# Kernel tuning notes

Measured on AMD Instinct MI355X. Metric: run time of the kernel, lower is better.

## Reference

```python
import jax, jax.numpy as jnp
import numpy as np

N = 30000          # nodes
E = 480000         # directed edges (avg degree 16)
F_IN = 376         # num_features (hard-coded in module)
HID = 512          # nhid (hard-coded)
NEG_SLOPE = 0.2    # PyG GATConv default negative_slope


def _lin(k, fi, fo):
    return (jax.random.normal(k, (fi, fo), jnp.float32) / np.sqrt(fi)).astype(jnp.float32)


def setup_inputs() -> dict:
    key = jax.random.key(0)
    ks = jax.random.split(key, 16)
    d = {}
    d["x"] = jax.random.normal(ks[0], (N, F_IN), jnp.float32)
    d["edge_index"] = jax.random.randint(ks[1], (2, E), 0, N)
    d["edge_weight"] = jax.random.uniform(ks[2], (E,), jnp.float32)
    # GCNConv(376,512) and GCNConv(512,512)
    d["W1"] = _lin(ks[3], F_IN, HID); d["b1"] = jnp.zeros((HID,), jnp.float32)
    d["W2"] = _lin(ks[4], HID, HID);  d["b2"] = jnp.zeros((HID,), jnp.float32)
    # SAGEConv(512,512): lin_l on aggregated neighbors, lin_r on root
    d["sage_Wl"] = _lin(ks[5], HID, HID)
    d["sage_Wr"] = _lin(ks[6], HID, HID)
    d["sage_b"] = jnp.zeros((HID,), jnp.float32)
    # GATConv(1536, 1, heads=4, concat=False)
    d["gat1_W"] = _lin(ks[7], 3 * HID, 4)
    d["gat1_a_src"] = jax.random.normal(ks[8], (4,), jnp.float32) * 0.1
    d["gat1_a_dst"] = jax.random.normal(ks[9], (4,), jnp.float32) * 0.1
    d["gat1_b"] = jnp.zeros((1,), jnp.float32)
    # GATConv(1536, 1, heads=16, concat=False)
    d["gat2_W"] = _lin(ks[10], 3 * HID, 16)
    d["gat2_a_src"] = jax.random.normal(ks[11], (16,), jnp.float32) * 0.1
    d["gat2_a_dst"] = jax.random.normal(ks[12], (16,), jnp.float32) * 0.1
    d["gat2_b"] = jnp.zeros((1,), jnp.float32)
    return d


def gcn_conv(x, src, dst, ew, W, b, n):
    # PyG GCNConv: add self-loops (weight 1), symmetric normalization
    loop = jnp.arange(n)
    s = jnp.concatenate([src, loop])
    t = jnp.concatenate([dst, loop])
    w = jnp.concatenate([ew, jnp.ones((n,), ew.dtype)])
    deg = jax.ops.segment_sum(w, t, num_segments=n)
    dinv = jnp.where(deg > 0, jax.lax.rsqrt(deg), 0.0)
    norm = dinv[s] * w * dinv[t]                       # [E+N]
    h = x @ W                                           # [N, out]
    out = jax.ops.segment_sum(norm[:, None] * h[s], t, num_segments=n)
    return out + b


def sage_conv(x, src, dst, Wl, Wr, b, n):
    # PyG SAGEConv: mean neighbor aggregation + root transform
    sums = jax.ops.segment_sum(x[src], dst, num_segments=n)
    cnt = jax.ops.segment_sum(jnp.ones((src.shape[0],), x.dtype), dst, num_segments=n)
    mean = sums / jnp.maximum(cnt, 1.0)[:, None]
    return mean @ Wl + x @ Wr + b


def gat_conv(x, src, dst, W, a_src, a_dst, b, n):
    # PyG GATConv (out_channels=1, concat=False -> mean over heads), self-loops added
    loop = jnp.arange(n)
    s = jnp.concatenate([src, loop])
    t = jnp.concatenate([dst, loop])
    h = x @ W                                           # [N, heads] (C=1)
    e = jax.nn.leaky_relu(h[s] * a_src + h[t] * a_dst, NEG_SLOPE)  # [E+N, heads]
    m = jax.ops.segment_max(e, t, num_segments=n)       # stable segment softmax
    ex = jnp.exp(e - m[t])
    den = jax.ops.segment_sum(ex, t, num_segments=n)
    alpha = ex / den[t]
    out = jax.ops.segment_sum(alpha * h[s], t, num_segments=n)     # [N, heads]
    return out.mean(axis=1, keepdims=True) + b          # [N, 1]


def reference(x, edge_index, edge_weight, W1, b1, W2, b2,
              sage_Wl, sage_Wr, sage_b,
              gat1_W, gat1_a_src, gat1_a_dst, gat1_b,
              gat2_W, gat2_a_src, gat2_a_dst, gat2_b):
    n = x.shape[0]
    src, dst = edge_index[0], edge_index[1]
    x1 = jax.nn.relu(gcn_conv(x, src, dst, edge_weight, W1, b1, n))
    x2 = jax.nn.relu(gcn_conv(x1, src, dst, edge_weight, W2, b2, n))
    x3 = jax.nn.relu(sage_conv(x1, src, dst, sage_Wl, sage_Wr, sage_b, n))
    dense_features = jnp.concatenate([x1, x2, x3], axis=1)  # [N, 1536]
    a1 = gat_conv(dense_features, src, dst, gat1_W, gat1_a_src, gat1_a_dst, gat1_b, n)
    a2 = gat_conv(dense_features, src, dst, gat2_W, gat2_a_src, gat2_a_dst, gat2_b, n)
    x_out = jnp.ravel((a1 + a2) * 0.5)                  # [N]
    return x_out, dense_features
```

## Files before the change

kernel.cpp:

```cpp
#include <hip/hip_runtime.h>
#include <hip/hip_bf16.h>
#include <stdint.h>

#define N_NODES 30000
#define M_PAD   30080
#define N_EDGES 480000
#define F_IN 376
#define K1   384
#define HID 512
#define DENSE_F 1536
#define NHEADS 20
#define HG_LD 128

typedef __bf16 bf16_t;
typedef bf16_t bf16x8 __attribute__((ext_vector_type(8)));
typedef bf16_t bf16x4 __attribute__((ext_vector_type(4)));
typedef float  f32x4  __attribute__((ext_vector_type(4)));

__global__ __launch_bounds__(256) void build_stats(
    const int* __restrict__ dst, const float* __restrict__ ew,
    float* __restrict__ deg, int* __restrict__ cnt)
{
    int e = blockIdx.x * 256 + threadIdx.x;
    if (e >= N_EDGES) return;
    int t = dst[e];
    atomicAdd(&deg[t], ew[e]);
    atomicAdd(&cnt[t], 1);
}

__global__ __launch_bounds__(256) void node_stats(
    float* __restrict__ deg, float* __restrict__ dinv)
{
    int i = blockIdx.x * 256 + threadIdx.x;
    if (i >= N_NODES) return;
    float d = deg[i] + 1.0f;
    deg[i] = d;
    dinv[i] = rsqrtf(d);
}

__global__ __launch_bounds__(1024) void scan_rowptr(
    const int* __restrict__ cnt, int* __restrict__ rowptr, int* __restrict__ woff)
{
    __shared__ int temp[1024];
    __shared__ int carry;
    int t = threadIdx.x;
    if (t == 0) carry = 0;
    __syncthreads();
    for (int base = 0; base < N_NODES; base += 1024) {
        int i = base + t;
        int v = (i < N_NODES) ? cnt[i] : 0;
        temp[t] = v;
        __syncthreads();
        for (int off = 1; off < 1024; off <<= 1) {
            int add = (t >= off) ? temp[t - off] : 0;
            __syncthreads();
            temp[t] += add;
            __syncthreads();
        }
        int excl = temp[t] - v;
        if (i < N_NODES) { rowptr[i] = carry + excl; woff[i] = carry + excl; }
        __syncthreads();
        if (t == 1023) carry += temp[1023];
        __syncthreads();
    }
    if (t == 0) rowptr[N_NODES] = carry;
}

__global__ __launch_bounds__(256) void scatter_csr(
    const int* __restrict__ src, const int* __restrict__ dst,
    const float* __restrict__ ew, int* __restrict__ woff,
    int* __restrict__ col, float* __restrict__ wcsr)
{
    int e = blockIdx.x * 256 + threadIdx.x;
    if (e >= N_EDGES) return;
    int t = dst[e];
    int p = atomicAdd(&woff[t], 1);
    col[p] = src[e];
    wcsr[p] = ew[e];
}

__global__ __launch_bounds__(256) void conv_x(
    const float* __restrict__ x, bf16_t* __restrict__ xb)
{
    int tid = blockIdx.x * 256 + threadIdx.x;
    if (tid >= M_PAD * K1) return;
    int r = tid / K1, c = tid - r * K1;
    float v = (r < N_NODES && c < F_IN) ? x[r * F_IN + c] : 0.f;
    xb[tid] = (bf16_t)v;
}

#define S1 (512 * K1)
#define S2 (512 * 512)
#define S3 (512 * 1024)
#define S4 (HG_LD * DENSE_F)
__global__ __launch_bounds__(256) void pack_weights(
    const float* __restrict__ W1, const float* __restrict__ W2,
    const float* __restrict__ Wl, const float* __restrict__ Wr,
    const float* __restrict__ g1W, const float* __restrict__ g2W,
    const float* __restrict__ a1s, const float* __restrict__ a1d,
    const float* __restrict__ a2s, const float* __restrict__ a2d,
    bf16_t* __restrict__ W1t, bf16_t* __restrict__ W2t,
    bf16_t* __restrict__ Bst, bf16_t* __restrict__ Wgt,
    float* __restrict__ asrc, float* __restrict__ adst)
{
    int tid = blockIdx.x * 256 + threadIdx.x;
    if (tid < S1) {
        int n = tid / K1, k = tid - n * K1;
        W1t[tid] = (bf16_t)((k < F_IN) ? W1[k * HID + n] : 0.f);
    } else if (tid < S1 + S2) {
        int t = tid - S1;
        int n = t >> 9, k = t & 511;
        W2t[t] = (bf16_t)W2[k * HID + n];
    } else if (tid < S1 + S2 + S3) {
        int t = tid - S1 - S2;
        int n = t >> 10, k = t & 1023;
        Bst[t] = (bf16_t)((k < HID) ? Wl[k * HID + n] : Wr[(k - HID) * HID + n]);
    } else if (tid < S1 + S2 + S3 + S4) {
        int t = tid - S1 - S2 - S3;
        int n = t / DENSE_F, k = t - n * DENSE_F;
        float v = (n < 4) ? g1W[k * 4 + n] : (n < NHEADS) ? g2W[k * 16 + (n - 4)] : 0.f;
        Wgt[t] = (bf16_t)v;
    } else if (tid < S1 + S2 + S3 + S4 + NHEADS) {
        int hh = tid - S1 - S2 - S3 - S4;
        asrc[hh] = (hh < 4) ? a1s[hh] : a2s[hh - 4];
        adst[hh] = (hh < 4) ? a1d[hh] : a2d[hh - 4];
    }
}

__global__ __launch_bounds__(256) void gemm_bf16(
    const bf16_t* __restrict__ A1, int lda1, int ksplit,
    const bf16_t* __restrict__ A2, int lda2,
    const bf16_t* __restrict__ Bt, int ldb,
    float* __restrict__ C, bf16_t* __restrict__ Cb, long ldc, int K)
{
    __shared__ bf16_t As[128 * 32];
    __shared__ bf16_t Bs[128 * 32];
    const int tid = threadIdx.x;
    const int wid = tid >> 6, lane = tid & 63;
    const int li = lane & 15, kq = lane >> 4;
    const int wm = (wid >> 1) * 64, wn = (wid & 1) * 64;
    const long r0 = (long)blockIdx.y * 128;
    const long n0 = (long)blockIdx.x * 128;

    f32x4 acc[4][4] = {};

    const int s0 = wid * 64 + lane;
    const int s1 = 256 + s0;
    const int am0 = s0 >> 2, ak0 = (s0 & 3) ^ ((am0 >> 1) & 3);
    const int am1 = s1 >> 2, ak1 = (s1 & 3) ^ ((am1 >> 1) & 3);
    const int swz = (li >> 1) & 3;

    for (int k0 = 0; k0 < K; k0 += 32) {
        const bf16_t* Ab; int lda;
        if (k0 < ksplit) { Ab = A1 + k0;            lda = lda1; }
        else             { Ab = A2 + (k0 - ksplit); lda = lda2; }
        __builtin_amdgcn_global_load_lds(
            (const __attribute__((address_space(1))) void*)(Ab + (r0 + am0) * (long)lda + ak0 * 8),
            (__attribute__((address_space(3))) void*)(As + (wid * 64) * 8), 16, 0, 0);
        __builtin_amdgcn_global_load_lds(
            (const __attribute__((address_space(1))) void*)(Ab + (r0 + am1) * (long)lda + ak1 * 8),
            (__attribute__((address_space(3))) void*)(As + (256 + wid * 64) * 8), 16, 0, 0);
        __builtin_amdgcn_global_load_lds(
            (const __attribute__((address_space(1))) void*)(Bt + (n0 + am0) * (long)ldb + k0 + ak0 * 8),
            (__attribute__((address_space(3))) void*)(Bs + (wid * 64) * 8), 16, 0, 0);
        __builtin_amdgcn_global_load_lds(
            (const __attribute__((address_space(1))) void*)(Bt + (n0 + am1) * (long)ldb + k0 + ak1 * 8),
            (__attribute__((address_space(3))) void*)(Bs + (256 + wid * 64) * 8), 16, 0, 0);
        __syncthreads();

        bf16x8 a[4], b[4];
#pragma unroll
        for (int f = 0; f < 4; ++f) {
            int m = wm + f * 16 + li;
            a[f] = *(const bf16x8*)(As + m * 32 + ((kq ^ swz) * 8));
            int n = wn + f * 16 + li;
            b[f] = *(const bf16x8*)(Bs + n * 32 + ((kq ^ swz) * 8));
        }
#pragma unroll
        for (int fm = 0; fm < 4; ++fm)
#pragma unroll
            for (int fn = 0; fn < 4; ++fn)
                acc[fm][fn] = __builtin_amdgcn_mfma_f32_16x16x32_bf16(
                    a[fm], b[fn], acc[fm][fn], 0, 0, 0);
        __syncthreads();
    }

    if (Cb) {
#pragma unroll
        for (int fm = 0; fm < 4; ++fm)
#pragma unroll
            for (int r = 0; r < 4; ++r) {
                long row = r0 + wm + fm * 16 + kq * 4 + r;
                bf16_t* cp = Cb + row * ldc + n0 + wn + li;
#pragma unroll
                for (int fn = 0; fn < 4; ++fn)
                    cp[fn * 16] = (bf16_t)acc[fm][fn][r];
            }
    } else {
#pragma unroll
        for (int fm = 0; fm < 4; ++fm)
#pragma unroll
            for (int r = 0; r < 4; ++r) {
                long row = r0 + wm + fm * 16 + kq * 4 + r;
                float* cp = C + row * ldc + n0 + wn + li;
#pragma unroll
                for (int fn = 0; fn < 4; ++fn)
                    cp[fn * 16] = acc[fm][fn][r];
            }
    }
}

__global__ __launch_bounds__(64) void gcn_agg(
    const bf16_t* __restrict__ hb, const int* __restrict__ rowptr,
    const int* __restrict__ col, const float* __restrict__ wcsr,
    const float* __restrict__ dinv, const float* __restrict__ deg,
    const float* __restrict__ bias, float* __restrict__ out,
    bf16_t* __restrict__ outb)
{
    int i = blockIdx.x;
    int c = threadIdx.x * 8;
    float di = dinv[i];
    float selfw = 1.0f / deg[i];
    bf16x8 sv = *(const bf16x8*)(hb + (long)i * HID + c);
    float acc0[8], acc1[8];
#pragma unroll
    for (int j = 0; j < 8; ++j) { acc0[j] = selfw * (float)sv[j]; acc1[j] = 0.f; }
    int e = rowptr[i], e1 = rowptr[i + 1];
    for (; e + 1 < e1; e += 2) {
        int sA = col[e], sB = col[e + 1];
        float wA = dinv[sA] * wcsr[e] * di;
        float wB = dinv[sB] * wcsr[e + 1] * di;
        bf16x8 vA = *(const bf16x8*)(hb + (long)sA * HID + c);
        bf16x8 vB = *(const bf16x8*)(hb + (long)sB * HID + c);
#pragma unroll
        for (int j = 0; j < 8; ++j) {
            acc0[j] = fmaf(wA, (float)vA[j], acc0[j]);
            acc1[j] = fmaf(wB, (float)vB[j], acc1[j]);
        }
    }
    if (e < e1) {
        int sA = col[e];
        float wA = dinv[sA] * wcsr[e] * di;
        bf16x8 vA = *(const bf16x8*)(hb + (long)sA * HID + c);
#pragma unroll
        for (int j = 0; j < 8; ++j) acc0[j] = fmaf(wA, (float)vA[j], acc0[j]);
    }
    float o[8];
#pragma unroll
    for (int j = 0; j < 8; ++j)
        o[j] = fmaxf(acc0[j] + acc1[j] + bias[c + j], 0.f);
    float* op = out + (long)i * DENSE_F + c;
    *reinterpret_cast<float4*>(op)     = make_float4(o[0], o[1], o[2], o[3]);
    *reinterpret_cast<float4*>(op + 4) = make_float4(o[4], o[5], o[6], o[7]);
    bf16x8 ob;
#pragma unroll
    for (int j = 0; j < 8; ++j) ob[j] = (bf16_t)o[j];
    *reinterpret_cast<bf16x8*>(outb + (long)i * DENSE_F + c) = ob;
}

__global__ __launch_bounds__(64) void sage_mean(
    const bf16_t* __restrict__ x1b, const int* __restrict__ rowptr,
    const int* __restrict__ col, const int* __restrict__ cnt,
    bf16_t* __restrict__ meanb)
{
    int i = blockIdx.x;
    int c = threadIdx.x * 8;
    float acc0[8] = {}, acc1[8] = {};
    int e = rowptr[i], e1 = rowptr[i + 1];
    for (; e + 1 < e1; e += 2) {
        int sA = col[e], sB = col[e + 1];
        bf16x8 vA = *(const bf16x8*)(x1b + (long)sA * DENSE_F + c);
        bf16x8 vB = *(const bf16x8*)(x1b + (long)sB * DENSE_F + c);
#pragma unroll
        for (int j = 0; j < 8; ++j) {
            acc0[j] += (float)vA[j];
            acc1[j] += (float)vB[j];
        }
    }
    if (e < e1) {
        int sA = col[e];
        bf16x8 vA = *(const bf16x8*)(x1b + (long)sA * DENSE_F + c);
#pragma unroll
        for (int j = 0; j < 8; ++j) acc0[j] += (float)vA[j];
    }
    float inv = 1.0f / fmaxf((float)cnt[i], 1.0f);
    bf16x8 ob;
#pragma unroll
    for (int j = 0; j < 8; ++j) ob[j] = (bf16_t)((acc0[j] + acc1[j]) * inv);
    *reinterpret_cast<bf16x8*>(meanb + (long)i * HID + c) = ob;
}

__global__ __launch_bounds__(256) void sage_finish(
    const float* __restrict__ h, const float* __restrict__ bias,
    float* __restrict__ out, bf16_t* __restrict__ outb)
{
    int tid = blockIdx.x * 256 + threadIdx.x;
    if (tid >= N_NODES * HID) return;
    int i = tid >> 9;
    int c = tid & (HID - 1);
    float v = fmaxf(h[tid] + bias[c], 0.f);
    out[(long)i * DENSE_F + c] = v;
    outb[(long)i * DENSE_F + c] = (bf16_t)v;
}

__global__ __launch_bounds__(64) void gat_agg(
    const float* __restrict__ hgat, const int* __restrict__ rowptr,
    const int* __restrict__ col, const float* __restrict__ asrc,
    const float* __restrict__ adst, const float* __restrict__ b1p,
    const float* __restrict__ b2p, float* __restrict__ xout)
{
    int i = blockIdx.x;
    int lane = threadIdx.x;
    int h = (lane < NHEADS) ? lane : 0;
    float hg_i = hgat[(long)i * HG_LD + h];
    float as = asrc[h], ad = adst[h];
    float adhg = ad * hg_i;
    float ev = hg_i * as + adhg;
    ev = ev > 0.f ? ev : 0.2f * ev;
    float ex = __expf(ev);
    float den = ex, og = ex * hg_i;
    int e0 = rowptr[i], e1 = rowptr[i + 1];
    for (int e = e0; e < e1; ++e) {
        int s = col[e];
        float hs = hgat[(long)s * HG_LD + h];
        float t = fmaf(hs, as, adhg);
        t = t > 0.f ? t : 0.2f * t;
        float x = __expf(t);
        den += x;
        og = fmaf(x, hs, og);
    }
    float out = (lane < NHEADS) ? og / den : 0.f;
    float s4 = out + __shfl_xor(out, 1);
    s4 += __shfl_xor(s4, 2);
    float g0 = __shfl(s4, 0);
    float g1 = __shfl(s4, 4);
    float g2 = __shfl(s4, 8);
    float g3 = __shfl(s4, 12);
    float g4 = __shfl(s4, 16);
    if (lane == 0) {
        float a1 = g0 * 0.25f + b1p[0];
        float a2 = (g1 + g2 + g3 + g4) * 0.0625f + b2p[0];
        xout[i] = 0.5f * (a1 + a2);
    }
}

extern "C" void kernel_launch(void* const* d_in, const int* in_sizes, int n_in,
                              void* d_out, int out_size, void* d_ws, size_t ws_size,
                              hipStream_t stream) {
    (void)in_sizes; (void)n_in; (void)out_size; (void)ws_size;
    const float* x    = (const float*)d_in[0];
    const int*   ei   = (const int*)d_in[1];
    const float* ew   = (const float*)d_in[2];
    const float* W1   = (const float*)d_in[3];
    const float* b1   = (const float*)d_in[4];
    const float* W2   = (const float*)d_in[5];
    const float* b2   = (const float*)d_in[6];
    const float* sWl  = (const float*)d_in[7];
    const float* sWr  = (const float*)d_in[8];
    const float* sb   = (const float*)d_in[9];
    const float* g1W  = (const float*)d_in[10];
    const float* g1as = (const float*)d_in[11];
    const float* g1ad = (const float*)d_in[12];
    const float* g1b  = (const float*)d_in[13];
    const float* g2W  = (const float*)d_in[14];
    const float* g2as = (const float*)d_in[15];
    const float* g2ad = (const float*)d_in[16];
    const float* g2b  = (const float*)d_in[17];

    const int* src = ei;
    const int* dst = ei + N_EDGES;

    float* xout  = (float*)d_out;
    float* dense = xout + N_NODES;

    size_t off = 0;
    auto alloc = [&](size_t nbytes) -> void* {
        void* p = (char*)d_ws + off;
        off += (nbytes + 255) & ~(size_t)255;
        return p;
    };
    float*  h        = (float*)alloc((size_t)M_PAD * HID * 4);
    bf16_t* h_bf     = (bf16_t*)h;
    bf16_t* dense_bf = (bf16_t*)alloc((size_t)M_PAD * DENSE_F * 2);
    bf16_t* x_bf     = (bf16_t*)alloc((size_t)M_PAD * K1 * 2);
    bf16_t* mean_bf  = (bf16_t*)alloc((size_t)M_PAD * HID * 2);
    bf16_t* W1t      = (bf16_t*)alloc((size_t)512 * K1 * 2);
    bf16_t* W2t      = (bf16_t*)alloc((size_t)512 * 512 * 2);
    bf16_t* Bst      = (bf16_t*)alloc((size_t)512 * 1024 * 2);
    bf16_t* Wgt      = (bf16_t*)alloc((size_t)HG_LD * DENSE_F * 2);
    float*  deg      = (float*)alloc((size_t)N_NODES * 4);
    float*  dinv     = (float*)alloc((size_t)N_NODES * 4);
    float*  asrc     = (float*)alloc(32 * 4);
    float*  adst     = (float*)alloc(32 * 4);
    int*    cnt      = (int*)alloc((size_t)N_NODES * 4);
    int*    rowp     = (int*)alloc((size_t)(N_NODES + 1) * 4);
    int*    woff     = (int*)alloc((size_t)N_NODES * 4);
    int*    colx     = (int*)alloc((size_t)N_EDGES * 4);
    float*  wcsr     = (float*)alloc((size_t)N_EDGES * 4);
    float*  hgat     = h;

    const int EB = (N_EDGES + 255) / 256;
    const int NB = (N_NODES + 255) / 256;

    hipMemsetAsync(deg, 0, (size_t)N_NODES * 4, stream);
    hipMemsetAsync(cnt, 0, (size_t)N_NODES * 4, stream);
    build_stats<<<EB, 256, 0, stream>>>(dst, ew, deg, cnt);
    node_stats<<<NB, 256, 0, stream>>>(deg, dinv);
    scan_rowptr<<<1, 1024, 0, stream>>>(cnt, rowp, woff);
    scatter_csr<<<EB, 256, 0, stream>>>(src, dst, ew, woff, colx, wcsr);

    conv_x<<<(M_PAD * K1 + 255) / 256, 256, 0, stream>>>(x, x_bf);
    pack_weights<<<(S1 + S2 + S3 + S4 + NHEADS + 255) / 256, 256, 0, stream>>>(
        W1, W2, sWl, sWr, g1W, g2W, g1as, g1ad, g2as, g2ad,
        W1t, W2t, Bst, Wgt, asrc, adst);

    const dim3 gB(256);
    const dim3 g512(HID / 128, M_PAD / 128);
    const dim3 g128(1, M_PAD / 128);

    gemm_bf16<<<g512, gB, 0, stream>>>(x_bf, K1, K1, x_bf, K1, W1t, K1,
                                       nullptr, h_bf, HID, K1);
    gcn_agg<<<N_NODES, 64, 0, stream>>>(h_bf, rowp, colx, wcsr, dinv, deg, b1,
                                        dense, dense_bf);
    gemm_bf16<<<g512, gB, 0, stream>>>(dense_bf, DENSE_F, HID, dense_bf, DENSE_F,
                                       W2t, HID, nullptr, h_bf, HID, HID);
    gcn_agg<<<N_NODES, 64, 0, stream>>>(h_bf, rowp, colx, wcsr, dinv, deg, b2,
                                        dense + HID, dense_bf + HID);
    sage_mean<<<N_NODES, 64, 0, stream>>>(dense_bf, rowp, colx, cnt, mean_bf);
    gemm_bf16<<<g512, gB, 0, stream>>>(mean_bf, HID, HID, dense_bf, DENSE_F,
                                       Bst, 1024, h, nullptr, HID, 1024);
    sage_finish<<<(N_NODES * HID + 255) / 256, 256, 0, stream>>>(
        h, sb, dense + 2 * HID, dense_bf + 2 * HID);

    gemm_bf16<<<g128, gB, 0, stream>>>(dense_bf, DENSE_F, DENSE_F, dense_bf, DENSE_F,
                                       Wgt, DENSE_F, hgat, nullptr, HG_LD, DENSE_F);
    gat_agg<<<N_NODES, 64, 0, stream>>>(hgat, rowp, colx, asrc, adst, g1b, g2b, xout);
}
```

Before: 871.2 us.

## Aggregate before transform in GCN layers and fuse bias/ReLU into GEMM epilogue

Result: faster. 802.8 us (-7.8%).

```diff
diff --git a/kernel.cpp b/kernel.cpp
--- a/kernel.cpp
+++ b/kernel.cpp
@@ -10,11 +10,10 @@
 #define HID 512
 #define DENSE_F 1536
 #define NHEADS 20
-#define HG_LD 128
+#define HG_LD 32
 
 typedef __bf16 bf16_t;
 typedef bf16_t bf16x8 __attribute__((ext_vector_type(8)));
-typedef bf16_t bf16x4 __attribute__((ext_vector_type(4)));
 typedef float  f32x4  __attribute__((ext_vector_type(4)));
 
 __global__ __launch_bounds__(256) void build_stats(
@@ -92,7 +91,7 @@
 #define S1 (512 * K1)
 #define S2 (512 * 512)
 #define S3 (512 * 1024)
-#define S4 (HG_LD * DENSE_F)
+#define S4 (128 * DENSE_F)
 __global__ __launch_bounds__(256) void pack_weights(
     const float* __restrict__ W1, const float* __restrict__ W2,
     const float* __restrict__ Wl, const float* __restrict__ Wr,
@@ -131,7 +130,8 @@
     const bf16_t* __restrict__ A1, int lda1, int ksplit,
     const bf16_t* __restrict__ A2, int lda2,
     const bf16_t* __restrict__ Bt, int ldb,
-    float* __restrict__ C, bf16_t* __restrict__ Cb, long ldc, int K)
+    float* __restrict__ C, bf16_t* __restrict__ Cb, long ldc, int K,
+    const float* __restrict__ bias, int ncols)
 {
     __shared__ bf16_t As[128 * 32];
     __shared__ bf16_t Bs[128 * 32];
@@ -140,7 +140,7 @@
     const int li = lane & 15, kq = lane >> 4;
     const int wm = (wid >> 1) * 64, wn = (wid & 1) * 64;
     const long r0 = (long)blockIdx.y * 128;
-    const long n0 = (long)blockIdx.x * 128;
+    const int  n0 = blockIdx.x * 128;
 
     f32x4 acc[4][4] = {};
 
@@ -185,122 +185,128 @@
         __syncthreads();
     }
 
-    if (Cb) {
-#pragma unroll
-        for (int fm = 0; fm < 4; ++fm)
-#pragma unroll
-            for (int r = 0; r < 4; ++r) {
-                long row = r0 + wm + fm * 16 + kq * 4 + r;
-                bf16_t* cp = Cb + row * ldc + n0 + wn + li;
-#pragma unroll
-                for (int fn = 0; fn < 4; ++fn)
-                    cp[fn * 16] = (bf16_t)acc[fm][fn][r];
+#pragma unroll
+    for (int fm = 0; fm < 4; ++fm) {
+#pragma unroll
+        for (int r = 0; r < 4; ++r) {
+            long row = r0 + wm + fm * 16 + kq * 4 + r;
+            if (row >= N_NODES) continue;
+#pragma unroll
+            for (int fn = 0; fn < 4; ++fn) {
+                int colg = n0 + wn + fn * 16 + li;
+                if (colg >= ncols) continue;
+                float v = acc[fm][fn][r];
+                if (bias) v = fmaxf(v + bias[colg], 0.f);
+                if (C)  C[row * ldc + colg]  = v;
+                if (Cb) Cb[row * ldc + colg] = (bf16_t)v;
             }
-    } else {
-#pragma unroll
-        for (int fm = 0; fm < 4; ++fm)
-#pragma unroll
-            for (int r = 0; r < 4; ++r) {
-                long row = r0 + wm + fm * 16 + kq * 4 + r;
-                float* cp = C + row * ldc + n0 + wn + li;
-#pragma unroll
-                for (int fn = 0; fn < 4; ++fn)
-                    cp[fn * 16] = acc[fm][fn][r];
-            }
-    }
-}
-
-__global__ __launch_bounds__(64) void gcn_agg(
-    const bf16_t* __restrict__ hb, const int* __restrict__ rowptr,
+        }
+    }
+}
+
+__global__ __launch_bounds__(64) void agg_x(
+    const bf16_t* __restrict__ xb, const int* __restrict__ rowptr,
     const int* __restrict__ col, const float* __restrict__ wcsr,
     const float* __restrict__ dinv, const float* __restrict__ deg,
-    const float* __restrict__ bias, float* __restrict__ out,
-    bf16_t* __restrict__ outb)
+    bf16_t* __restrict__ aggx)
 {
     int i = blockIdx.x;
     int c = threadIdx.x * 8;
+    bool act = (c < K1);
     float di = dinv[i];
     float selfw = 1.0f / deg[i];
-    bf16x8 sv = *(const bf16x8*)(hb + (long)i * HID + c);
-    float acc0[8], acc1[8];
-#pragma unroll
-    for (int j = 0; j < 8; ++j) { acc0[j] = selfw * (float)sv[j]; acc1[j] = 0.f; }
+    float acc0[8] = {}, acc1[8] = {};
+    if (act) {
+        bf16x8 sv = *(const bf16x8*)(xb + (long)i * K1 + c);
+#pragma unroll
+        for (int j = 0; j < 8; ++j) acc0[j] = selfw * (float)sv[j];
+    }
     int e = rowptr[i], e1 = rowptr[i + 1];
     for (; e + 1 < e1; e += 2) {
         int sA = col[e], sB = col[e + 1];
         float wA = dinv[sA] * wcsr[e] * di;
         float wB = dinv[sB] * wcsr[e + 1] * di;
-        bf16x8 vA = *(const bf16x8*)(hb + (long)sA * HID + c);
-        bf16x8 vB = *(const bf16x8*)(hb + (long)sB * HID + c);
-#pragma unroll
-        for (int j = 0; j < 8; ++j) {
-            acc0[j] = fmaf(wA, (float)vA[j], acc0[j]);
-            acc1[j] = fmaf(wB, (float)vB[j], acc1[j]);
+        if (act) {
+            bf16x8 vA = *(const bf16x8*)(xb + (long)sA * K1 + c);
+            bf16x8 vB = *(const bf16x8*)(xb + (long)sB * K1 + c);
+#pragma unroll
+            for (int j = 0; j < 8; ++j) {
+                acc0[j] = fmaf(wA, (float)vA[j], acc0[j]);
+                acc1[j] = fmaf(wB, (float)vB[j], acc1[j]);
+            }
         }
     }
     if (e < e1) {
         int sA = col[e];
         float wA = dinv[sA] * wcsr[e] * di;
-        bf16x8 vA = *(const bf16x8*)(hb + (long)sA * HID + c);
-#pragma unroll
-        for (int j = 0; j < 8; ++j) acc0[j] = fmaf(wA, (float)vA[j], acc0[j]);
-    }
-    float o[8];
-#pragma unroll
-    for (int j = 0; j < 8; ++j)
-        o[j] = fmaxf(acc0[j] + acc1[j] + bias[c + j], 0.f);
-    float* op = out + (long)i * DENSE_F + c;
-    *reinterpret_cast<float4*>(op)     = make_float4(o[0], o[1], o[2], o[3]);
-    *reinterpret_cast<float4*>(op + 4) = make_float4(o[4], o[5], o[6], o[7]);
-    bf16x8 ob;
-#pragma unroll
-    for (int j = 0; j < 8; ++j) ob[j] = (bf16_t)o[j];
-    *reinterpret_cast<bf16x8*>(outb + (long)i * DENSE_F + c) = ob;
-}
-
-__global__ __launch_bounds__(64) void sage_mean(
-    const bf16_t* __restrict__ x1b, const int* __restrict__ rowptr,
-    const int* __restrict__ col, const int* __restrict__ cnt,
-    bf16_t* __restrict__ meanb)
+        if (act) {
+            bf16x8 vA = *(const bf16x8*)(xb + (long)sA * K1 + c);
+#pragma unroll
+            for (int j = 0; j < 8; ++j) acc0[j] = fmaf(wA, (float)vA[j], acc0[j]);
+        }
+    }
+    if (act) {
+        bf16x8 ob;
+#pragma unroll
+        for (int j = 0; j < 8; ++j) ob[j] = (bf16_t)(acc0[j] + acc1[j]);
+        *reinterpret_cast<bf16x8*>(aggx + (long)i * K1 + c) = ob;
+    }
+}
+
+__global__ __launch_bounds__(64) void agg_x1(
+    const bf16_t* __restrict__ x1b ,
+    const int* __restrict__ rowptr, const int* __restrict__ col,
+    const float* __restrict__ wcsr, const float* __restrict__ dinv,
+    const float* __restrict__ deg, const int* __restrict__ cnt,
+    bf16_t* __restrict__ gbf, bf16_t* __restrict__ meanb)
 {
     int i = blockIdx.x;
     int c = threadIdx.x * 8;
-    float acc0[8] = {}, acc1[8] = {};
+    float di = dinv[i];
+    float selfw = 1.0f / deg[i];
+    bf16x8 sv = *(const bf16x8*)(x1b + (long)i * DENSE_F + c);
+    float g0[8], g1[8], m0[8], m1[8];
+#pragma unroll
+    for (int j = 0; j < 8; ++j) {
+        g0[j] = selfw * (float)sv[j];
+        g1[j] = 0.f; m0[j] = 0.f; m1[j] = 0.f;
+    }
     int e = rowptr[i], e1 = rowptr[i + 1];
     for (; e + 1 < e1; e += 2) {
         int sA = col[e], sB = col[e + 1];
+        float wA = dinv[sA] * wcsr[e] * di;
+        float wB = dinv[sB] * wcsr[e + 1] * di;
         bf16x8 vA = *(const bf16x8*)(x1b + (long)sA * DENSE_F + c);
         bf16x8 vB = *(const bf16x8*)(x1b + (long)sB * DENSE_F + c);
 #pragma unroll
         for (int j = 0; j < 8; ++j) {
-            acc0[j] += (float)vA[j];
-            acc1[j] += (float)vB[j];
+            float fA = (float)vA[j], fB = (float)vB[j];
+            g0[j] = fmaf(wA, fA, g0[j]);
+            g1[j] = fmaf(wB, fB, g1[j]);
+            m0[j] += fA;
+            m1[j] += fB;
         }
     }
     if (e < e1) {
         int sA = col[e];
+        float wA = dinv[sA] * wcsr[e] * di;
         bf16x8 vA = *(const bf16x8*)(x1b + (long)sA * DENSE_F + c);
 #pragma unroll
-        for (int j = 0; j < 8; ++j) acc0[j] += (float)vA[j];
+        for (int j = 0; j < 8; ++j) {
+            float fA = (float)vA[j];
+            g0[j] = fmaf(wA, fA, g0[j]);
+            m0[j] += fA;
+        }
     }
     float inv = 1.0f / fmaxf((float)cnt[i], 1.0f);
-    bf16x8 ob;
-#pragma unroll
-    for (int j = 0; j < 8; ++j) ob[j] = (bf16_t)((acc0[j] + acc1[j]) * inv);
-    *reinterpret_cast<bf16x8*>(meanb + (long)i * HID + c) = ob;
-}
-
-__global__ __launch_bounds__(256) void sage_finish(
-    const float* __restrict__ h, const float* __restrict__ bias,
-    float* __restrict__ out, bf16_t* __restrict__ outb)
-{
-    int tid = blockIdx.x * 256 + threadIdx.x;
-    if (tid >= N_NODES * HID) return;
-    int i = tid >> 9;
-    int c = tid & (HID - 1);
-    float v = fmaxf(h[tid] + bias[c], 0.f);
-    out[(long)i * DENSE_F + c] = v;
-    outb[(long)i * DENSE_F + c] = (bf16_t)v;
+    bf16x8 og, om;
+#pragma unroll
+    for (int j = 0; j < 8; ++j) {
+        og[j] = (bf16_t)(g0[j] + g1[j]);
+        om[j] = (bf16_t)((m0[j] + m1[j]) * inv);
+    }
+    *reinterpret_cast<bf16x8*>(gbf   + (long)i * HID + c) = og;
+    *reinterpret_cast<bf16x8*>(meanb + (long)i * HID + c) = om;
 }
 
 __global__ __launch_bounds__(64) void gat_agg(
@@ -318,18 +324,26 @@
     float ev = hg_i * as + adhg;
     ev = ev > 0.f ? ev : 0.2f * ev;
     float ex = __expf(ev);
-    float den = ex, og = ex * hg_i;
-    int e0 = rowptr[i], e1 = rowptr[i + 1];
-    for (int e = e0; e < e1; ++e) {
-        int s = col[e];
-        float hs = hgat[(long)s * HG_LD + h];
-        float t = fmaf(hs, as, adhg);
-        t = t > 0.f ? t : 0.2f * t;
-        float x = __expf(t);
-        den += x;
-        og = fmaf(x, hs, og);
-    }
-    float out = (lane < NHEADS) ? og / den : 0.f;
+    float den0 = ex, og0 = ex * hg_i, den1 = 0.f, og1 = 0.f;
+    int e = rowptr[i], e1 = rowptr[i + 1];
+    for (; e + 1 < e1; e += 2) {
+        int sA = col[e], sB = col[e + 1];
+        float hA = hgat[(long)sA * HG_LD + h];
+        float hB = hgat[(long)sB * HG_LD + h];
+        float tA = fmaf(hA, as, adhg); tA = tA > 0.f ? tA : 0.2f * tA;
+        float tB = fmaf(hB, as, adhg); tB = tB > 0.f ? tB : 0.2f * tB;
+        float xA = __expf(tA), xB = __expf(tB);
+        den0 += xA; og0 = fmaf(xA, hA, og0);
+        den1 += xB; og1 = fmaf(xB, hB, og1);
+    }
+    if (e < e1) {
+        int sA = col[e];
+        float hA = hgat[(long)sA * HG_LD + h];
+        float tA = fmaf(hA, as, adhg); tA = tA > 0.f ? tA : 0.2f * tA;
+        float xA = __expf(tA);
+        den0 += xA; og0 = fmaf(xA, hA, og0);
+    }
+    float out = (lane < NHEADS) ? (og0 + og1) / (den0 + den1) : 0.f;
     float s4 = out + __shfl_xor(out, 1);
     s4 += __shfl_xor(s4, 2);
     float g0 = __shfl(s4, 0);
@@ -379,15 +393,16 @@
         off += (nbytes + 255) & ~(size_t)255;
         return p;
     };
-    float*  h        = (float*)alloc((size_t)M_PAD * HID * 4);
-    bf16_t* h_bf     = (bf16_t*)h;
     bf16_t* dense_bf = (bf16_t*)alloc((size_t)M_PAD * DENSE_F * 2);
     bf16_t* x_bf     = (bf16_t*)alloc((size_t)M_PAD * K1 * 2);
+    bf16_t* aggx_bf  = (bf16_t*)alloc((size_t)M_PAD * K1 * 2);
+    bf16_t* g_bf     = (bf16_t*)alloc((size_t)M_PAD * HID * 2);
     bf16_t* mean_bf  = (bf16_t*)alloc((size_t)M_PAD * HID * 2);
+    float*  hgat     = (float*)alloc((size_t)M_PAD * HG_LD * 4);
     bf16_t* W1t      = (bf16_t*)alloc((size_t)512 * K1 * 2);
     bf16_t* W2t      = (bf16_t*)alloc((size_t)512 * 512 * 2);
     bf16_t* Bst      = (bf16_t*)alloc((size_t)512 * 1024 * 2);
-    bf16_t* Wgt      = (bf16_t*)alloc((size_t)HG_LD * DENSE_F * 2);
+    bf16_t* Wgt      = (bf16_t*)alloc((size_t)128 * DENSE_F * 2);
     float*  deg      = (float*)alloc((size_t)N_NODES * 4);
     float*  dinv     = (float*)alloc((size_t)N_NODES * 4);
     float*  asrc     = (float*)alloc(32 * 4);
@@ -397,7 +412,6 @@
     int*    woff     = (int*)alloc((size_t)N_NODES * 4);
     int*    colx     = (int*)alloc((size_t)N_EDGES * 4);
     float*  wcsr     = (float*)alloc((size_t)N_EDGES * 4);
-    float*  hgat     = h;
 
     const int EB = (N_EDGES + 255) / 256;
     const int NB = (N_NODES + 255) / 256;
@@ -418,21 +432,21 @@
     const dim3 g512(HID / 128, M_PAD / 128);
     const dim3 g128(1, M_PAD / 128);
 
-    gemm_bf16<<<g512, gB, 0, stream>>>(x_bf, K1, K1, x_bf, K1, W1t, K1,
-                                       nullptr, h_bf, HID, K1);
-    gcn_agg<<<N_NODES, 64, 0, stream>>>(h_bf, rowp, colx, wcsr, dinv, deg, b1,
-                                        dense, dense_bf);
-    gemm_bf16<<<g512, gB, 0, stream>>>(dense_bf, DENSE_F, HID, dense_bf, DENSE_F,
-                                       W2t, HID, nullptr, h_bf, HID, HID);
-    gcn_agg<<<N_NODES, 64, 0, stream>>>(h_bf, rowp, colx, wcsr, dinv, deg, b2,
-                                        dense + HID, dense_bf + HID);
-    sage_mean<<<N_NODES, 64, 0, stream>>>(dense_bf, rowp, colx, cnt, mean_bf);
+    agg_x<<<N_NODES, 64, 0, stream>>>(x_bf, rowp, colx, wcsr, dinv, deg, aggx_bf);
+    gemm_bf16<<<g512, gB, 0, stream>>>(aggx_bf, K1, K1, aggx_bf, K1, W1t, K1,
+                                       dense, dense_bf, DENSE_F, K1, b1, 512);
+
+    agg_x1<<<N_NODES, 64, 0, stream>>>(dense_bf, rowp, colx, wcsr, dinv, deg, cnt,
+                                       g_bf, mean_bf);
+    gemm_bf16<<<g512, gB, 0, stream>>>(g_bf, HID, HID, g_bf, HID, W2t, HID,
+                                       dense + HID, dense_bf + HID, DENSE_F,
+                                       HID, b2, 512);
     gemm_bf16<<<g512, gB, 0, stream>>>(mean_bf, HID, HID, dense_bf, DENSE_F,
-                                       Bst, 1024, h, nullptr, HID, 1024);
-    sage_finish<<<(N_NODES * HID + 255) / 256, 256, 0, stream>>>(
-        h, sb, dense + 2 * HID, dense_bf + 2 * HID);
+                                       Bst, 1024, dense + 2 * HID,
+                                       dense_bf + 2 * HID, DENSE_F, 1024, sb, 512);
 
     gemm_bf16<<<g128, gB, 0, stream>>>(dense_bf, DENSE_F, DENSE_F, dense_bf, DENSE_F,
-                                       Wgt, DENSE_F, hgat, nullptr, HG_LD, DENSE_F);
+                                       Wgt, DENSE_F, hgat, nullptr, HG_LD,
+                                       DENSE_F, nullptr, HG_LD);
     gat_agg<<<N_NODES, 64, 0, stream>>>(hgat, rowp, colx, asrc, adst, g1b, g2b, xout);
 }
```
